# Kernel tuning notes

Hardware: AMD Instinct MI355X
Metric: run time of the kernel (lower is better)

The kernel has to match this reference:

```python
import jax, jax.numpy as jnp
import numpy as np

E = 8
D_IN = 1024
D_HID = 4096
D_OUT = 1024
T = 16384  # total tokens, equally split: 2048 per expert


def setup_inputs() -> dict:
    key = jax.random.key(0)
    k1, k2, k3, k4, k5 = jax.random.split(key, 5)
    x = jax.random.normal(k1, (T, D_IN), dtype=jnp.float32)
    cnt = jnp.full((E,), T // E, dtype=jnp.int32)  # tokens per expert (sorted/contiguous)
    s1 = 1.0 / np.sqrt(D_IN)
    s2 = 1.0 / np.sqrt(D_HID)
    w1 = jax.random.uniform(k2, (E, D_HID, D_IN), jnp.float32, -s1, s1)
    b1 = jax.random.uniform(k3, (E, D_HID), jnp.float32, -s1, s1)
    w2 = jax.random.uniform(k4, (E, D_OUT, D_HID), jnp.float32, -s2, s2)
    b2 = jax.random.uniform(k5, (E, D_OUT), jnp.float32, -s2, s2)
    return {"x": x, "cnt": cnt, "w1": w1, "b1": b1, "w2": w2, "b2": b2}


def reference(x, cnt, w1, b1, w2, b2):
    # FMoELinear: tokens are laid out contiguously by expert per `cnt`.
    # With equal counts (T // E per expert) the grouped GEMM is a batched einsum.
    e = w1.shape[0]
    t, d = x.shape
    cap = t // e  # tokens per expert
    xg = x.reshape(e, cap, d)                               # [E, cap, d_in]
    h = jnp.einsum('ecd,ehd->ech', xg, w1) + b1[:, None, :]  # fc1: [E, cap, d_hid]
    h = jax.nn.gelu(h, approximate=False)                    # nn.GELU (exact erf)
    # drop1 / drop2 are p=0.0 (identity); sub_norm is Identity (use_subln=False)
    y = jnp.einsum('ech,eoh->eco', h, w2) + b2[:, None, :]   # fc2: [E, cap, d_out]
    return y.reshape(t, -1)
```

## Files before the change

### kernel.cpp

```cpp
#include <hip/hip_runtime.h>
#include <hip/hip_bf16.h>
#include <cstdint>

#define NUM_E 8
#define DIN   1024
#define DHID  4096
#define DOUTP 1024
#define TTOK  16384
#define CAP   2048

typedef __attribute__((ext_vector_type(8))) short bf16x8;
typedef __attribute__((ext_vector_type(4))) float f32x4;

static __device__ __forceinline__ ushort f32_to_bf16_rne(float f) {
  uint32_t b = __float_as_uint(f);
  b += 0x7fffu + ((b >> 16) & 1u);
  return (ushort)(b >> 16);
}

static __device__ __forceinline__ float erf_fast(float x) {
  const float ax = __builtin_fabsf(x);
  const float t  = __builtin_amdgcn_rcpf(__builtin_fmaf(0.3275911f, ax, 1.0f));
  float p = __builtin_fmaf(1.061405429f, t, -1.453152027f);
  p = __builtin_fmaf(p, t, 1.421413741f);
  p = __builtin_fmaf(p, t, -0.284496736f);
  p = __builtin_fmaf(p, t, 0.254829592f);
  p = p * t;
  const float e = __expf(-ax * ax);
  const float r = __builtin_fmaf(-p, e, 1.0f);
  return __builtin_copysignf(r, x);
}

static __device__ __forceinline__ void cvt8(const float* __restrict__ in,
                                            ushort* __restrict__ out) {
  float4 a = *reinterpret_cast<const float4*>(in);
  float4 b = *reinterpret_cast<const float4*>(in + 4);
  union { ushort u[8]; uint4 v; } o;
  o.u[0] = f32_to_bf16_rne(a.x); o.u[1] = f32_to_bf16_rne(a.y);
  o.u[2] = f32_to_bf16_rne(a.z); o.u[3] = f32_to_bf16_rne(a.w);
  o.u[4] = f32_to_bf16_rne(b.x); o.u[5] = f32_to_bf16_rne(b.y);
  o.u[6] = f32_to_bf16_rne(b.z); o.u[7] = f32_to_bf16_rne(b.w);
  *reinterpret_cast<uint4*>(out) = o.v;
}

__global__ void __launch_bounds__(256) cvt2_bf16_kernel(
    const float* __restrict__ in1, ushort* __restrict__ out1, unsigned n1,
    const float* __restrict__ in2, ushort* __restrict__ out2, unsigned n2) {
  const unsigned stride = gridDim.x * 256u * 8u;
  for (unsigned i = (blockIdx.x * 256u + threadIdx.x) * 8u; i < n1; i += stride)
    cvt8(in1 + i, out1 + i);
  for (unsigned i = (blockIdx.x * 256u + threadIdx.x) * 8u; i < n2; i += stride)
    cvt8(in2 + i, out2 + i);
}

#define GLD(g, l)                                                                 \
  __builtin_amdgcn_global_load_lds((const __attribute__((address_space(1))) void*)(g), \
                                   (__attribute__((address_space(3))) void*)(l), 16, 0, 0)

template <int K, int N, int TILES_N, bool GELU_BF16_OUT, bool CVT_W2>
__global__ void __launch_bounds__(512, 1) grouped_gemm_kernel(
    const ushort* __restrict__ A,
    const ushort* __restrict__ B,
    const float* __restrict__ bias,
    void* __restrict__ Cout,
    const float* __restrict__ cvt_src,
    ushort* __restrict__ cvt_dst) {
  constexpr int TILES_M = CAP / 256;
  constexpr int BPE = TILES_M * TILES_N;
  constexpr int NT = K / 64;
  constexpr int NTI = NT / 2;
  static_assert(NT >= 4 && (NT & 1) == 0, "need even NT >= 4");

  __shared__ uint8_t lds[131072];

  const int tid = (blockIdx.x & 7) * BPE + (blockIdx.x >> 3);
  const int e   = tid / BPE;
  const int rm  = tid % BPE;
  const int nt  = rm / TILES_M;
  const int mt  = rm % TILES_M;

  const int t  = threadIdx.x;
  const int w  = t >> 6, l = t & 63;
  const int wm = w >> 2, wn = w & 3;
  const int lr = l & 15;
  const int kg = l >> 4;
  const int col0 = nt * 256 + wn * 64;

  const int gr  = t >> 3;
  const int sch = (t & 7) ^ (gr & 7);
  const ushort* gA = A + ((long)(e * CAP + mt * 256) + gr) * K + sch * 8;
  const ushort* gB = B + ((long)(e * N) + nt * 256 + gr) * K + sch * 8;
  uint8_t* const dT = lds + t * 16;

#define SA(j, h) { const ushort* s_ = gA + (long)(h) * 128 * K + (long)(j) * 64;   \
    uint8_t* d_ = dT + (((j) & 1) << 16) + ((h) << 14);                            \
    GLD(s_, d_); GLD(s_ + (long)64 * K, d_ + 8192); }
#define SB(j, h) { const ushort* s_ = gB + (long)(h) * 128 * K + (long)(j) * 64;   \
    uint8_t* d_ = dT + (((j) & 1) << 16) + 32768 + ((h) << 14);                    \
    GLD(s_, d_); GLD(s_ + (long)64 * K, d_ + 8192); }

  int offA[8][2], offB[4][2];
#pragma unroll
  for (int m = 0; m < 8; ++m) {
    const int r = m * 16 + lr;
#pragma unroll
    for (int kh = 0; kh < 2; ++kh)
      offA[m][kh] = r * 128 + ((((kh << 2) | kg) ^ (r & 7)) << 4);
  }
#pragma unroll
  for (int n = 0; n < 4; ++n) {
    const int r = (wn & 1) * 64 + n * 16 + lr;
#pragma unroll
    for (int kh = 0; kh < 2; ++kh)
      offB[n][kh] = r * 128 + ((((kh << 2) | kg) ^ (r & 7)) << 4);
  }
  const int rdAoff = wm << 14;
  const int rdBoff = 32768 + ((wn >> 1) << 14);

  f32x4 acc[8][4] = {};

  SA(0, 0); SA(0, 1); SB(0, 0); SB(0, 1);
  SB(1, 0); SB(1, 1);
  asm volatile("s_waitcnt vmcnt(4)" ::: "memory");
  __builtin_amdgcn_s_barrier();

#define PHASE_MFMA(AF, BF, AI, NI)                                                 \
    __builtin_amdgcn_s_barrier();                                                  \
    asm volatile("s_waitcnt lgkmcnt(0)" ::: "memory");                             \
    __builtin_amdgcn_sched_barrier(0);                                             \
    __builtin_amdgcn_s_setprio(1);                                                 \
    _Pragma("unroll")                                                              \
    for (int m = 0; m < 4; ++m)                                                    \
      _Pragma("unroll")                                                            \
      for (int n = 0; n < 2; ++n)                                                  \
        _Pragma("unroll")                                                          \
        for (int kh = 0; kh < 2; ++kh)                                             \
          acc[m + (AI)][n + (NI)] = __builtin_amdgcn_mfma_f32_16x16x32_bf16(       \
              AF[m][kh], BF[n][kh], acc[m + (AI)][n + (NI)], 0, 0, 0);             \
    __builtin_amdgcn_s_setprio(0);

#define RD_A0(SRC) _Pragma("unroll")                                               \
    for (int m = 0; m < 4; ++m) _Pragma("unroll")                                  \
      for (int kh = 0; kh < 2; ++kh)                                               \
        a0[m][kh] = *reinterpret_cast<const bf16x8*>((SRC) + offA[m][kh]);
#define RD_A1(SRC) _Pragma("unroll")                                               \
    for (int m = 0; m < 4; ++m) _Pragma("unroll")                                  \
      for (int kh = 0; kh < 2; ++kh)                                               \
        a1[m][kh] = *reinterpret_cast<const bf16x8*>((SRC) + offA[m + 4][kh]);
#define RD_B0(SRC) _Pragma("unroll")                                               \
    for (int n = 0; n < 2; ++n) _Pragma("unroll")                                  \
      for (int kh = 0; kh < 2; ++kh)                                               \
        b0[n][kh] = *reinterpret_cast<const bf16x8*>((SRC) + offB[n][kh]);
#define RD_B1(SRC) _Pragma("unroll")                                               \
    for (int n = 0; n < 2; ++n) _Pragma("unroll")                                  \
      for (int kh = 0; kh < 2; ++kh)                                               \
        b1[n][kh] = *reinterpret_cast<const bf16x8*>((SRC) + offB[n + 2][kh]);

  for (int i = 0; i < NTI; ++i) {
    const int u = 2 * i, v = u + 1;
    const bool st = (u + 2) < NT;
    const uint8_t* rA0 = lds + rdAoff;
    const uint8_t* rB0 = lds + rdBoff;
    const uint8_t* rA1 = lds + 65536 + rdAoff;
    const uint8_t* rB1 = lds + 65536 + rdBoff;
    bf16x8 a0[4][2], a1[4][2], b0[2][2], b1[2][2];

    RD_A0(rA0) RD_B0(rB0)
    SA(v, 0);
    PHASE_MFMA(a0, b0, 0, 0)
    __builtin_amdgcn_s_barrier();

    RD_B1(rB0)
    SA(v, 1);
    PHASE_MFMA(a0, b1, 0, 2)
    __builtin_amdgcn_s_barrier();

    RD_A1(rA0)
    if (st) SB(u + 2, 0);
    PHASE_MFMA(a1, b1, 4, 2)
    __builtin_amdgcn_s_barrier();

    if (st) SB(u + 2, 1);
    PHASE_MFMA(a1, b0, 4, 0)
    if (st) { asm volatile("s_waitcnt vmcnt(4)" ::: "memory"); }
    else    { asm volatile("s_waitcnt vmcnt(0)" ::: "memory"); }
    __builtin_amdgcn_s_barrier();

    RD_A0(rA1) RD_B0(rB1)
    if (st) SA(u + 2, 0);
    PHASE_MFMA(a0, b0, 0, 0)
    __builtin_amdgcn_s_barrier();

    RD_B1(rB1)
    if (st) SA(u + 2, 1);
    PHASE_MFMA(a0, b1, 0, 2)
    __builtin_amdgcn_s_barrier();

    RD_A1(rA1)
    if (st) SB(v + 2, 0);
    PHASE_MFMA(a1, b1, 4, 2)
    __builtin_amdgcn_s_barrier();

    if (st) SB(v + 2, 1);
    PHASE_MFMA(a1, b0, 4, 0)
    if (st) { asm volatile("s_waitcnt vmcnt(4)" ::: "memory"); }
    __builtin_amdgcn_s_barrier();
  }

  const long rowg0 = (long)e * CAP + mt * 256 + wm * 128;
  float bv[4];
#pragma unroll
  for (int n = 0; n < 4; ++n) bv[n] = bias[(long)e * N + col0 + n * 16 + lr];

  if constexpr (GELU_BF16_OUT) {
    uint8_t* const sl = lds + (w << 14);
#pragma unroll
    for (int n = 0; n < 4; ++n) {
#pragma unroll
      for (int m = 0; m < 8; ++m) {
#pragma unroll
        for (int q = 0; q < 4; ++q) {
          const int r = m * 16 + kg * 4 + q;
          const int c = n * 16 + lr;
          float vx = acc[m][n][q] + bv[n];
          vx = 0.5f * vx * (1.0f + erf_fast(vx * 0.70710678118654752f));
          *(ushort*)(sl + r * 128 + ((((c >> 3) ^ (r & 7))) << 4) + (c & 7) * 2) =
              f32_to_bf16_rne(vx);
        }
      }
    }
    asm volatile("s_waitcnt lgkmcnt(0)" ::: "memory");
    ushort* const Cb = (ushort*)Cout;
#pragma unroll
    for (int it = 0; it < 16; ++it) {
      const int idx = it * 64 + l;
      const int r = idx >> 3, c16 = idx & 7;
      uint4 vv = *reinterpret_cast<const uint4*>(sl + r * 128 + ((c16 ^ (r & 7)) << 4));
      *reinterpret_cast<uint4*>(Cb + (rowg0 + r) * N + col0 + c16 * 8) = vv;
    }
  } else {
    float* const Cf = (float*)Cout;
#pragma unroll
    for (int n = 0; n < 4; ++n) {
#pragma unroll
      for (int m = 0; m < 8; ++m) {
#pragma unroll
        for (int q = 0; q < 4; ++q) {
          const int r = m * 16 + kg * 4 + q;
          Cf[(rowg0 + r) * N + col0 + n * 16 + lr] = acc[m][n][q] + bv[n];
        }
      }
    }
  }

  if constexpr (CVT_W2) {
    const long base = (long)blockIdx.x * 32768;
#pragma unroll
    for (int it = 0; it < 8; ++it) {
      const long idx = base + (long)it * 4096 + t * 8;
      cvt8(cvt_src + idx, cvt_dst + idx);
    }
  }
#undef SA
#undef SB
#undef PHASE_MFMA
#undef RD_A0
#undef RD_A1
#undef RD_B0
#undef RD_B1
}

extern "C" void kernel_launch(void* const* d_in, const int* in_sizes, int n_in,
                              void* d_out, int out_size, void* d_ws, size_t ws_size,
                              hipStream_t stream) {
  const float* x  = (const float*)d_in[0];
  const float* w1 = (const float*)d_in[2];
  const float* b1 = (const float*)d_in[3];
  const float* w2 = (const float*)d_in[4];
  const float* b2 = (const float*)d_in[5];
  float* out = (float*)d_out;

  constexpr size_t W2B_OFF = 67108864;
  constexpr size_t HB_OFF  = 134217728;
  constexpr size_t WS_NEED = 268435456;
  if (ws_size < WS_NEED) return;

  ushort* w1b = (ushort*)d_ws;
  ushort* w2b = (ushort*)d_ws + W2B_OFF;
  ushort* hb  = (ushort*)d_ws + HB_OFF;
  ushort* xb  = (ushort*)d_out;

  cvt2_bf16_kernel<<<2048, 256, 0, stream>>>(
      x, xb, (unsigned)(TTOK * DIN), w1, w1b, (unsigned)(NUM_E * DHID * DIN));

  grouped_gemm_kernel<DIN, DHID, DHID / 256, true, true>
      <<<dim3(NUM_E * (CAP / 256) * (DHID / 256)), 512, 0, stream>>>(
          xb, w1b, b1, hb, w2, w2b);

  grouped_gemm_kernel<DHID, DOUTP, DOUTP / 256, false, false>
      <<<dim3(NUM_E * (CAP / 256) * (DOUTP / 256)), 512, 0, stream>>>(
          hb, w2b, b2, out, nullptr, nullptr);
}
```

Measured before the change: 353.2 us.

## Make fc1 GEMM persistent over four N-subtiles with cross-tile prefetch

The fc1 grouped GEMM now launches 256 blocks, one per CU, and each block walks four consecutive 256-wide N subtiles instead of launching one block per tile. During the last K iteration of a subtile it prefetches the next subtile's first A/B stages, so the next tile's loads overlap the current tile's MFMA tail and epilogue. The GELU epilogue is also reworked to stage through LDS in 32-row chunks in the second buffer, so it does not collide with the prefetched data. This removes the wave-quantization tail of 1024 blocks on 256 CUs and per-block ramp-up, but the A tile is re-fetched for each subtile, and the extra barriers plus LDS reuse add complexity.

```diff
diff --git a/kernel.cpp b/kernel.cpp
--- a/kernel.cpp
+++ b/kernel.cpp
@@ -57,7 +57,7 @@
   __builtin_amdgcn_global_load_lds((const __attribute__((address_space(1))) void*)(g), \
                                    (__attribute__((address_space(3))) void*)(l), 16, 0, 0)
 
-template <int K, int N, int TILES_N, bool GELU_BF16_OUT, bool CVT_W2>
+template <int K, int N, int TILES_N, int SUBT, bool GELU_BF16_OUT, bool CVT_W2>
 __global__ void __launch_bounds__(512, 1) grouped_gemm_kernel(
     const ushort* __restrict__ A,
     const ushort* __restrict__ B,
@@ -66,7 +66,8 @@
     const float* __restrict__ cvt_src,
     ushort* __restrict__ cvt_dst) {
   constexpr int TILES_M = CAP / 256;
-  constexpr int BPE = TILES_M * TILES_N;
+  constexpr int NTG = TILES_N / SUBT;
+  constexpr int BPE = TILES_M * NTG;
   constexpr int NT = K / 64;
   constexpr int NTI = NT / 2;
   static_assert(NT >= 4 && (NT & 1) == 0, "need even NT >= 4");
@@ -76,7 +77,7 @@
   const int tid = (blockIdx.x & 7) * BPE + (blockIdx.x >> 3);
   const int e   = tid / BPE;
   const int rm  = tid % BPE;
-  const int nt  = rm / TILES_M;
+  const int ntg = rm / TILES_M;
   const int mt  = rm % TILES_M;
 
   const int t  = threadIdx.x;
@@ -84,18 +85,17 @@
   const int wm = w >> 2, wn = w & 3;
   const int lr = l & 15;
   const int kg = l >> 4;
-  const int col0 = nt * 256 + wn * 64;
 
   const int gr  = t >> 3;
   const int sch = (t & 7) ^ (gr & 7);
-  const ushort* gA = A + ((long)(e * CAP + mt * 256) + gr) * K + sch * 8;
-  const ushort* gB = B + ((long)(e * N) + nt * 256 + gr) * K + sch * 8;
+  const ushort* gA  = A + ((long)(e * CAP + mt * 256) + gr) * K + sch * 8;
+  const ushort* gBb = B + ((long)(e * N) + ntg * (SUBT * 256) + gr) * K + sch * 8;
   uint8_t* const dT = lds + t * 16;
 
-#define SA(j, h) { const ushort* s_ = gA + (long)(h) * 128 * K + (long)(j) * 64;   \
+#define SA_(j, h) { const ushort* s_ = gA + (long)(h) * 128 * K + (long)(j) * 64;  \
     uint8_t* d_ = dT + (((j) & 1) << 16) + ((h) << 14);                            \
     GLD(s_, d_); GLD(s_ + (long)64 * K, d_ + 8192); }
-#define SB(j, h) { const ushort* s_ = gB + (long)(h) * 128 * K + (long)(j) * 64;   \
+#define SB_(p, j, h) { const ushort* s_ = (p) + (long)(h) * 128 * K + (long)(j) * 64; \
     uint8_t* d_ = dT + (((j) & 1) << 16) + 32768 + ((h) << 14);                    \
     GLD(s_, d_); GLD(s_ + (long)64 * K, d_ + 8192); }
 
@@ -118,11 +118,6 @@
   const int rdBoff = 32768 + ((wn >> 1) << 14);
 
   f32x4 acc[8][4] = {};
-
-  SA(0, 0); SA(0, 1); SB(0, 0); SB(0, 1);
-  SB(1, 0); SB(1, 1);
-  asm volatile("s_waitcnt vmcnt(4)" ::: "memory");
-  __builtin_amdgcn_s_barrier();
 
 #define PHASE_MFMA(AF, BF, AI, NI)                                                 \
     __builtin_amdgcn_s_barrier();                                                  \
@@ -156,113 +151,140 @@
       for (int kh = 0; kh < 2; ++kh)                                               \
         b1[n][kh] = *reinterpret_cast<const bf16x8*>((SRC) + offB[n + 2][kh]);
 
-  for (int i = 0; i < NTI; ++i) {
-    const int u = 2 * i, v = u + 1;
-    const bool st = (u + 2) < NT;
-    const uint8_t* rA0 = lds + rdAoff;
-    const uint8_t* rB0 = lds + rdBoff;
-    const uint8_t* rA1 = lds + 65536 + rdAoff;
-    const uint8_t* rB1 = lds + 65536 + rdBoff;
-    bf16x8 a0[4][2], a1[4][2], b0[2][2], b1[2][2];
-
-    RD_A0(rA0) RD_B0(rB0)
-    SA(v, 0);
-    PHASE_MFMA(a0, b0, 0, 0)
-    __builtin_amdgcn_s_barrier();
-
-    RD_B1(rB0)
-    SA(v, 1);
-    PHASE_MFMA(a0, b1, 0, 2)
-    __builtin_amdgcn_s_barrier();
-
-    RD_A1(rA0)
-    if (st) SB(u + 2, 0);
-    PHASE_MFMA(a1, b1, 4, 2)
-    __builtin_amdgcn_s_barrier();
-
-    if (st) SB(u + 2, 1);
-    PHASE_MFMA(a1, b0, 4, 0)
-    if (st) { asm volatile("s_waitcnt vmcnt(4)" ::: "memory"); }
-    else    { asm volatile("s_waitcnt vmcnt(0)" ::: "memory"); }
-    __builtin_amdgcn_s_barrier();
-
-    RD_A0(rA1) RD_B0(rB1)
-    if (st) SA(u + 2, 0);
-    PHASE_MFMA(a0, b0, 0, 0)
-    __builtin_amdgcn_s_barrier();
-
-    RD_B1(rB1)
-    if (st) SA(u + 2, 1);
-    PHASE_MFMA(a0, b1, 0, 2)
-    __builtin_amdgcn_s_barrier();
-
-    RD_A1(rA1)
-    if (st) SB(v + 2, 0);
-    PHASE_MFMA(a1, b1, 4, 2)
-    __builtin_amdgcn_s_barrier();
-
-    if (st) SB(v + 2, 1);
-    PHASE_MFMA(a1, b0, 4, 0)
-    if (st) { asm volatile("s_waitcnt vmcnt(4)" ::: "memory"); }
-    __builtin_amdgcn_s_barrier();
-  }
+  SA_(0, 0); SA_(0, 1); SB_(gBb, 0, 0); SB_(gBb, 0, 1);
+  SB_(gBb, 1, 0); SB_(gBb, 1, 1);
+  asm volatile("s_waitcnt vmcnt(4)" ::: "memory");
+  __builtin_amdgcn_s_barrier();
 
   const long rowg0 = (long)e * CAP + mt * 256 + wm * 128;
-  float bv[4];
-#pragma unroll
-  for (int n = 0; n < 4; ++n) bv[n] = bias[(long)e * N + col0 + n * 16 + lr];
-
-  if constexpr (GELU_BF16_OUT) {
-    uint8_t* const sl = lds + (w << 14);
-#pragma unroll
-    for (int n = 0; n < 4; ++n) {
-#pragma unroll
-      for (int m = 0; m < 8; ++m) {
-#pragma unroll
-        for (int q = 0; q < 4; ++q) {
-          const int r = m * 16 + kg * 4 + q;
-          const int c = n * 16 + lr;
-          float vx = acc[m][n][q] + bv[n];
-          vx = 0.5f * vx * (1.0f + erf_fast(vx * 0.70710678118654752f));
-          *(ushort*)(sl + r * 128 + ((((c >> 3) ^ (r & 7))) << 4) + (c & 7) * 2) =
-              f32_to_bf16_rne(vx);
+
+  for (int s = 0; s < SUBT; ++s) {
+    const ushort* gBs = gBb + (long)s * 256 * K;
+    const ushort* gBn = gBb + (long)(s + 1) * 256 * K;
+    const int col0 = (ntg * SUBT + s) * 256 + wn * 64;
+
+    float bv[4];
+#pragma unroll
+    for (int n = 0; n < 4; ++n) bv[n] = bias[(long)e * N + col0 + n * 16 + lr];
+
+    for (int i = 0; i < NTI; ++i) {
+      const int u = 2 * i, v = u + 1;
+      const bool stn = (i < NTI - 1);
+      const bool stx = (!stn) && (s + 1 < SUBT);
+      const uint8_t* rA0 = lds + rdAoff;
+      const uint8_t* rB0 = lds + rdBoff;
+      const uint8_t* rA1 = lds + 65536 + rdAoff;
+      const uint8_t* rB1 = lds + 65536 + rdBoff;
+      bf16x8 a0[4][2], a1[4][2], b0[2][2], b1[2][2];
+
+      RD_A0(rA0) RD_B0(rB0)
+      SA_(v, 0);
+      PHASE_MFMA(a0, b0, 0, 0)
+      __builtin_amdgcn_s_barrier();
+
+      RD_B1(rB0)
+      SA_(v, 1);
+      PHASE_MFMA(a0, b1, 0, 2)
+      __builtin_amdgcn_s_barrier();
+
+      RD_A1(rA0)
+      if (stn) { SB_(gBs, u + 2, 0); } else if (stx) { SB_(gBn, 0, 0); }
+      PHASE_MFMA(a1, b1, 4, 2)
+      __builtin_amdgcn_s_barrier();
+
+      if (stn) { SB_(gBs, u + 2, 1); } else if (stx) { SB_(gBn, 0, 1); }
+      PHASE_MFMA(a1, b0, 4, 0)
+      if (stn || stx) { asm volatile("s_waitcnt vmcnt(4)" ::: "memory"); }
+      else            { asm volatile("s_waitcnt vmcnt(0)" ::: "memory"); }
+      __builtin_amdgcn_s_barrier();
+
+      RD_A0(rA1) RD_B0(rB1)
+      if (stn) { SA_(u + 2, 0); } else if (stx) { SA_(0, 0); }
+      PHASE_MFMA(a0, b0, 0, 0)
+      __builtin_amdgcn_s_barrier();
+
+      RD_B1(rB1)
+      if (stn) { SA_(u + 2, 1); } else if (stx) { SA_(0, 1); }
+      PHASE_MFMA(a0, b1, 0, 2)
+      __builtin_amdgcn_s_barrier();
+
+      RD_A1(rA1)
+      if (stn) { SB_(gBs, v + 2, 0); } else if (stx) { SB_(gBn, 1, 0); }
+      PHASE_MFMA(a1, b1, 4, 2)
+      __builtin_amdgcn_s_barrier();
+
+      if (stn) { SB_(gBs, v + 2, 1); } else if (stx) { SB_(gBn, 1, 1); }
+      PHASE_MFMA(a1, b0, 4, 0)
+      if (stn || stx) { asm volatile("s_waitcnt vmcnt(4)" ::: "memory"); }
+      __builtin_amdgcn_s_barrier();
+    }
+
+    if constexpr (GELU_BF16_OUT) {
+      uint8_t* const sl = lds + 65536 + (w << 12);
+      ushort* const Cb = (ushort*)Cout;
+#pragma unroll
+      for (int p = 0; p < 4; ++p) {
+#pragma unroll
+        for (int m2 = 0; m2 < 2; ++m2) {
+#pragma unroll
+          for (int n = 0; n < 4; ++n) {
+#pragma unroll
+            for (int q = 0; q < 4; ++q) {
+              const int rr = m2 * 16 + kg * 4 + q;
+              const int c  = n * 16 + lr;
+              float vx = acc[2 * p + m2][n][q] + bv[n];
+              vx = 0.5f * vx * (1.0f + erf_fast(vx * 0.70710678118654752f));
+              *(ushort*)(sl + rr * 128 + (((c >> 3) ^ (rr & 7)) << 4) + (c & 7) * 2) =
+                  f32_to_bf16_rne(vx);
+            }
+          }
+        }
+        asm volatile("s_waitcnt lgkmcnt(0)" ::: "memory");
+        __builtin_amdgcn_sched_barrier(0);
+#pragma unroll
+        for (int j = 0; j < 4; ++j) {
+          const int idx = j * 64 + l;
+          const int rr = idx >> 3, c16 = idx & 7;
+          uint4 vv = *reinterpret_cast<const uint4*>(sl + rr * 128 + ((c16 ^ (rr & 7)) << 4));
+          *reinterpret_cast<uint4*>(Cb + (rowg0 + p * 32 + rr) * N + col0 + c16 * 8) = vv;
+        }
+        asm volatile("s_waitcnt lgkmcnt(0)" ::: "memory");
+        __builtin_amdgcn_sched_barrier(0);
+      }
+    } else {
+      float* const Cf = (float*)Cout;
+#pragma unroll
+      for (int n = 0; n < 4; ++n) {
+#pragma unroll
+        for (int m = 0; m < 8; ++m) {
+#pragma unroll
+          for (int q = 0; q < 4; ++q) {
+            const int r = m * 16 + kg * 4 + q;
+            Cf[(rowg0 + r) * N + col0 + n * 16 + lr] = acc[m][n][q] + bv[n];
+          }
         }
       }
     }
-    asm volatile("s_waitcnt lgkmcnt(0)" ::: "memory");
-    ushort* const Cb = (ushort*)Cout;
-#pragma unroll
-    for (int it = 0; it < 16; ++it) {
-      const int idx = it * 64 + l;
-      const int r = idx >> 3, c16 = idx & 7;
-      uint4 vv = *reinterpret_cast<const uint4*>(sl + r * 128 + ((c16 ^ (r & 7)) << 4));
-      *reinterpret_cast<uint4*>(Cb + (rowg0 + r) * N + col0 + c16 * 8) = vv;
+
+    if (s + 1 < SUBT) {
+      __builtin_amdgcn_s_barrier();
+#pragma unroll
+      for (int m = 0; m < 8; ++m)
+#pragma unroll
+        for (int n = 0; n < 4; ++n) acc[m][n] = f32x4{0.f, 0.f, 0.f, 0.f};
     }
-  } else {
-    float* const Cf = (float*)Cout;
-#pragma unroll
-    for (int n = 0; n < 4; ++n) {
-#pragma unroll
-      for (int m = 0; m < 8; ++m) {
-#pragma unroll
-        for (int q = 0; q < 4; ++q) {
-          const int r = m * 16 + kg * 4 + q;
-          Cf[(rowg0 + r) * N + col0 + n * 16 + lr] = acc[m][n][q] + bv[n];
-        }
+
+    if constexpr (CVT_W2) {
+      const long base = (long)blockIdx.x * (SUBT * 32768L) + (long)s * 32768;
+#pragma unroll
+      for (int it = 0; it < 8; ++it) {
+        const long idx = base + (long)it * 4096 + t * 8;
+        cvt8(cvt_src + idx, cvt_dst + idx);
       }
     }
   }
-
-  if constexpr (CVT_W2) {
-    const long base = (long)blockIdx.x * 32768;
-#pragma unroll
-    for (int it = 0; it < 8; ++it) {
-      const long idx = base + (long)it * 4096 + t * 8;
-      cvt8(cvt_src + idx, cvt_dst + idx);
-    }
-  }
-#undef SA
-#undef SB
+#undef SA_
+#undef SB_
 #undef PHASE_MFMA
 #undef RD_A0
 #undef RD_A1
@@ -293,11 +315,9 @@
   cvt2_bf16_kernel<<<2048, 256, 0, stream>>>(
       x, xb, (unsigned)(TTOK * DIN), w1, w1b, (unsigned)(NUM_E * DHID * DIN));
 
-  grouped_gemm_kernel<DIN, DHID, DHID / 256, true, true>
-      <<<dim3(NUM_E * (CAP / 256) * (DHID / 256)), 512, 0, stream>>>(
-          xb, w1b, b1, hb, w2, w2b);
-
-  grouped_gemm_kernel<DHID, DOUTP, DOUTP / 256, false, false>
-      <<<dim3(NUM_E * (CAP / 256) * (DOUTP / 256)), 512, 0, stream>>>(
-          hb, w2b, b2, out, nullptr, nullptr);
-}
+  grouped_gemm_kernel<DIN, DHID, DHID / 256, 4, true, true>
+      <<<dim3(256), 512, 0, stream>>>(xb, w1b, b1, hb, w2, w2b);
+
+  grouped_gemm_kernel<DHID, DOUTP, DOUTP / 256, 1, false, false>
+      <<<dim3(256), 512, 0, stream>>>(hb, w2b, b2, out, nullptr, nullptr);
+}
```

Result: slower. 382.6 us (+8.3%).

## Split global-to-LDS loads finer and prefetch next tiles earlier; batch W2 conversion loads

Applied to the files above, without the earlier changes.

Global-to-LDS prefetches are split into half-tile units, and the A tile for step u+2 now begins loading one phase earlier, during the current iteration. The wait threshold rises from vmcnt 4 to 6 so more loads stay in flight across barriers. The fused W2 fp32-to-bf16 conversion now issues all its global loads before the LDS-to-global output copy and does the conversion afterwards, so load latency overlaps the store. This raises register pressure from 16 float4s and prefetch depth, and the exact vmcnt accounting must stay correct to avoid races.

```diff
diff --git a/kernel.cpp b/kernel.cpp
--- a/kernel.cpp
+++ b/kernel.cpp
@@ -69,7 +69,7 @@
   constexpr int BPE = TILES_M * TILES_N;
   constexpr int NT = K / 64;
   constexpr int NTI = NT / 2;
-  static_assert(NT >= 4 && (NT & 1) == 0, "need even NT >= 4");
+  static_assert(NT >= 6 && (NT & 1) == 0, "need even NT >= 6");
 
   __shared__ uint8_t lds[131072];
 
@@ -92,12 +92,10 @@
   const ushort* gB = B + ((long)(e * N) + nt * 256 + gr) * K + sch * 8;
   uint8_t* const dT = lds + t * 16;
 
-#define SA(j, h) { const ushort* s_ = gA + (long)(h) * 128 * K + (long)(j) * 64;   \
-    uint8_t* d_ = dT + (((j) & 1) << 16) + ((h) << 14);                            \
-    GLD(s_, d_); GLD(s_ + (long)64 * K, d_ + 8192); }
-#define SB(j, h) { const ushort* s_ = gB + (long)(h) * 128 * K + (long)(j) * 64;   \
-    uint8_t* d_ = dT + (((j) & 1) << 16) + 32768 + ((h) << 14);                    \
-    GLD(s_, d_); GLD(s_ + (long)64 * K, d_ + 8192); }
+#define SAU(j, h, s) GLD(gA + (long)((h) * 128 + (s) * 64) * K + (long)(j) * 64,   \
+                         dT + (((j) & 1) << 16) + ((h) << 14) + ((s) << 13))
+#define SBU(j, h, s) GLD(gB + (long)((h) * 128 + (s) * 64) * K + (long)(j) * 64,   \
+                         dT + (((j) & 1) << 16) + 32768 + ((h) << 14) + ((s) << 13))
 
   int offA[8][2], offB[4][2];
 #pragma unroll
@@ -119,9 +117,11 @@
 
   f32x4 acc[8][4] = {};
 
-  SA(0, 0); SA(0, 1); SB(0, 0); SB(0, 1);
-  SB(1, 0); SB(1, 1);
-  asm volatile("s_waitcnt vmcnt(4)" ::: "memory");
+  SAU(0, 0, 0); SAU(0, 0, 1); SAU(0, 1, 0); SAU(0, 1, 1);
+  SBU(0, 0, 0); SBU(0, 0, 1); SBU(0, 1, 0); SBU(0, 1, 1);
+  SAU(1, 0, 0); SAU(1, 1, 0);
+  SBU(1, 0, 0); SBU(1, 0, 1); SBU(1, 1, 0); SBU(1, 1, 1);
+  asm volatile("s_waitcnt vmcnt(6)" ::: "memory");
   __builtin_amdgcn_s_barrier();
 
 #define PHASE_MFMA(AF, BF, AI, NI)                                                 \
@@ -166,44 +166,44 @@
     bf16x8 a0[4][2], a1[4][2], b0[2][2], b1[2][2];
 
     RD_A0(rA0) RD_B0(rB0)
-    SA(v, 0);
+    SAU(v, 0, 1); SAU(v, 1, 1);
     PHASE_MFMA(a0, b0, 0, 0)
     __builtin_amdgcn_s_barrier();
 
     RD_B1(rB0)
-    SA(v, 1);
+    if (st) { SAU(u + 2, 0, 0); SAU(u + 2, 1, 0); }
     PHASE_MFMA(a0, b1, 0, 2)
     __builtin_amdgcn_s_barrier();
 
     RD_A1(rA0)
-    if (st) SB(u + 2, 0);
+    if (st) { SBU(u + 2, 0, 0); SBU(u + 2, 0, 1); }
     PHASE_MFMA(a1, b1, 4, 2)
     __builtin_amdgcn_s_barrier();
 
-    if (st) SB(u + 2, 1);
+    if (st) { SBU(u + 2, 1, 0); SBU(u + 2, 1, 1); }
     PHASE_MFMA(a1, b0, 4, 0)
-    if (st) { asm volatile("s_waitcnt vmcnt(4)" ::: "memory"); }
+    if (st) { asm volatile("s_waitcnt vmcnt(6)" ::: "memory"); }
     else    { asm volatile("s_waitcnt vmcnt(0)" ::: "memory"); }
     __builtin_amdgcn_s_barrier();
 
     RD_A0(rA1) RD_B0(rB1)
-    if (st) SA(u + 2, 0);
+    if (st) { SAU(u + 2, 0, 1); SAU(u + 2, 1, 1); }
     PHASE_MFMA(a0, b0, 0, 0)
     __builtin_amdgcn_s_barrier();
 
     RD_B1(rB1)
-    if (st) SA(u + 2, 1);
+    if (st) { SAU(v + 2, 0, 0); SAU(v + 2, 1, 0); }
     PHASE_MFMA(a0, b1, 0, 2)
     __builtin_amdgcn_s_barrier();
 
     RD_A1(rA1)
-    if (st) SB(v + 2, 0);
+    if (st) { SBU(v + 2, 0, 0); SBU(v + 2, 0, 1); }
     PHASE_MFMA(a1, b1, 4, 2)
     __builtin_amdgcn_s_barrier();
 
-    if (st) SB(v + 2, 1);
+    if (st) { SBU(v + 2, 1, 0); SBU(v + 2, 1, 1); }
     PHASE_MFMA(a1, b0, 4, 0)
-    if (st) { asm volatile("s_waitcnt vmcnt(4)" ::: "memory"); }
+    if (st) { asm volatile("s_waitcnt vmcnt(6)" ::: "memory"); }
     __builtin_amdgcn_s_barrier();
   }
 
@@ -230,6 +230,18 @@
       }
     }
     asm volatile("s_waitcnt lgkmcnt(0)" ::: "memory");
+
+    float4 cv[16];
+    long cvbase = 0;
+    if constexpr (CVT_W2) {
+      cvbase = (long)blockIdx.x * 32768 + t * 8;
+#pragma unroll
+      for (int it = 0; it < 8; ++it) {
+        cv[2 * it]     = *reinterpret_cast<const float4*>(cvt_src + cvbase + (long)it * 4096);
+        cv[2 * it + 1] = *reinterpret_cast<const float4*>(cvt_src + cvbase + (long)it * 4096 + 4);
+      }
+    }
+
     ushort* const Cb = (ushort*)Cout;
 #pragma unroll
     for (int it = 0; it < 16; ++it) {
@@ -238,6 +250,19 @@
       uint4 vv = *reinterpret_cast<const uint4*>(sl + r * 128 + ((c16 ^ (r & 7)) << 4));
       *reinterpret_cast<uint4*>(Cb + (rowg0 + r) * N + col0 + c16 * 8) = vv;
     }
+
+    if constexpr (CVT_W2) {
+#pragma unroll
+      for (int it = 0; it < 8; ++it) {
+        union { ushort u[8]; uint4 v; } o;
+        const float4 a = cv[2 * it], b = cv[2 * it + 1];
+        o.u[0] = f32_to_bf16_rne(a.x); o.u[1] = f32_to_bf16_rne(a.y);
+        o.u[2] = f32_to_bf16_rne(a.z); o.u[3] = f32_to_bf16_rne(a.w);
+        o.u[4] = f32_to_bf16_rne(b.x); o.u[5] = f32_to_bf16_rne(b.y);
+        o.u[6] = f32_to_bf16_rne(b.z); o.u[7] = f32_to_bf16_rne(b.w);
+        *reinterpret_cast<uint4*>(cvt_dst + cvbase + (long)it * 4096) = o.v;
+      }
+    }
   } else {
     float* const Cf = (float*)Cout;
 #pragma unroll
@@ -252,17 +277,8 @@
       }
     }
   }
-
-  if constexpr (CVT_W2) {
-    const long base = (long)blockIdx.x * 32768;
-#pragma unroll
-    for (int it = 0; it < 8; ++it) {
-      const long idx = base + (long)it * 4096 + t * 8;
-      cvt8(cvt_src + idx, cvt_dst + idx);
-    }
-  }
-#undef SA
-#undef SB
+#undef SAU
+#undef SBU
 #undef PHASE_MFMA
 #undef RD_A0
 #undef RD_A1
```

After: 352.7 us (median of 2 runs). About the same (-0.1%).
